# Kernel tuning notes

Hardware: AMD Instinct MI355X
Metric: run time of the kernel (lower is better)

The kernel has to match this reference:

```python
import jax, jax.numpy as jnp
import numpy as np

N = 131072
N_DIM = 128
NUM_LAYERS = 8
N_MID = NUM_LAYERS - 2  # middle (n_dim -> n_dim) layers


def _sigmoid_layer(h, u_un, w_un, log_a, b):
    # h: [N, in]; u_un: [out, in]; w_un: [out, out]; log_a, b: [out, 1]
    a = jnp.exp(log_a)                      # [out, 1]
    u = jax.nn.softmax(u_un, axis=1)        # row-softmax, matches Softmax(dim=1)
    w = jax.nn.softmax(w_un, axis=1)
    inner = h @ (a * u).T + b[:, 0]         # [N, out]
    return jax.nn.sigmoid(inner) @ w.T      # [N, out]


def setup_inputs() -> dict:
    key = jax.random.key(0)
    ks = jax.random.split(key, 24)
    d = N_DIM
    inp = {
        "x": jax.random.normal(ks[0], (N,), jnp.float32),
        "fy0": jax.random.normal(ks[1], (N,), jnp.float32),
        # first layer (in=2, out=d)
        "u0": jax.random.normal(ks[2], (d, 2), jnp.float32),
        "w0": jax.random.normal(ks[3], (d, d), jnp.float32),
        "la0": jax.random.normal(ks[4], (d, 1), jnp.float32),
        "b0": jax.random.normal(ks[5], (d, 1), jnp.float32),
        # middle layers stacked (in=d, out=d)
        "uM": jax.random.normal(ks[6], (N_MID, d, d), jnp.float32),
        "wM": jax.random.normal(ks[7], (N_MID, d, d), jnp.float32),
        "laM": jax.random.normal(ks[8], (N_MID, d, 1), jnp.float32),
        "bM": jax.random.normal(ks[9], (N_MID, d, 1), jnp.float32),
        # last layer (in=d, out=1)
        "uL": jax.random.normal(ks[10], (1, d), jnp.float32),
        "wL": jax.random.normal(ks[11], (1, 1), jnp.float32),
        "laL": jax.random.normal(ks[12], (1, 1), jnp.float32),
        "bL": jax.random.normal(ks[13], (1, 1), jnp.float32),
        # MLP 1 -> 50 -> 50 -> 1
        "W1": jax.random.normal(ks[14], (50, 1), jnp.float32) * 0.2,
        "b1": jax.random.normal(ks[15], (50,), jnp.float32) * 0.2,
        "W2": jax.random.normal(ks[16], (50, 50), jnp.float32) * 0.1,
        "b2": jax.random.normal(ks[17], (50,), jnp.float32) * 0.1,
        "W3": jax.random.normal(ks[18], (1, 50), jnp.float32) * 0.1,
        "b3": jax.random.normal(ks[19], (1,), jnp.float32) * 0.1,
    }
    return inp


def reference(x, fy0, u0, w0, la0, b0, uM, wM, laM, bM, uL, wL, laL, bL,
              W1, b1, W2, b2, W3, b3):
    # MLP feature net on fy0: [N,1] -> [N,1]
    h = jax.nn.relu(fy0[:, None] @ W1.T + b1)
    h = jax.nn.relu(h @ W2.T + b2)
    theta = h @ W3.T + b3                          # [N, 1]
    mono = jnp.concatenate([x[:, None], theta], 1)  # [N, 2]

    mono = _sigmoid_layer(mono, u0, w0, la0, b0)    # [N, d]

    def step(carry, p):
        u_un, w_un, log_a, b = p
        return _sigmoid_layer(carry, u_un, w_un, log_a, b), None

    mono, _ = jax.lax.scan(step, mono, (uM, wM, laM, bM))
    out = _sigmoid_layer(mono, uL, wL, laL, bL)     # [N, 1]
    return out[:, :, None]                          # [N, 1, 1] matches torch
```

## Files before the change

kernel.cpp:

```cpp
#include <hip/hip_runtime.h>
#include <cstdint>

typedef __attribute__((ext_vector_type(8))) _Float16 half8;
typedef __attribute__((ext_vector_type(16))) float f32x16;
typedef __attribute__((ext_vector_type(4))) float f4;

#define LOG2E 1.44269504088896340f
#define KNL  (-1.44269504088896340f)

__device__ __forceinline__ float fast_exp(float x) { return __builtin_amdgcn_exp2f(LOG2E * x); }
__device__ __forceinline__ float sigmoidf(float v) {
    return __builtin_amdgcn_rcpf(1.f + __builtin_amdgcn_exp2f(KNL * v));
}
__device__ __forceinline__ float sig2(float y) {
    return __builtin_amdgcn_rcpf(1.f + __builtin_amdgcn_exp2f(y));
}
__device__ __forceinline__ unsigned pkz(float a, float b) {
    return __builtin_bit_cast(unsigned, __builtin_amdgcn_cvt_pkrtz(a, b));
}
__device__ __forceinline__ void swapl(unsigned& a, unsigned& b) {
    asm volatile("v_permlane32_swap_b32 %0, %1" : "+v"(a), "+v"(b));
}
__device__ __forceinline__ void swaplf(float& a, float& b) {
    asm volatile("v_permlane32_swap_b32 %0, %1" : "+v"(a), "+v"(b));
}
union BU { unsigned u[4]; half8 h; };

constexpr int A0X = 0, A0T = 128, B0O = 256, BMO = 384, VLO = 1152,
              W1P = 1280, B1P = 1344, B2P = 1408, W3P = 1472, CN = 1536;

constexpr int LSTRIDE = 40960;
constexpr int GOFF  = 0;
constexpr int W2HIO = 6 * LSTRIDE;
constexpr int W2LOO = W2HIO + 8192;
constexpr int CGOFF = W2LOO + 8192;

__device__ __forceinline__ int rank_desc(const float* __restrict__ la, int i) {
    float mv = la[i];
    int r = 0;
    for (int j = 0; j < 128; ++j) {
        float v = la[j];
        r += (v > mv) || (v == mv && j < i);
    }
    return r;
}

__global__ __launch_bounds__(256)
void prep_kernel(const float* __restrict__ u0, const float* __restrict__ w0,
                 const float* __restrict__ la0, const float* __restrict__ b0,
                 const float* __restrict__ uM, const float* __restrict__ wM,
                 const float* __restrict__ laM, const float* __restrict__ bM,
                 const float* __restrict__ uL, const float* __restrict__ laL,
                 const float* __restrict__ W1, const float* __restrict__ b1,
                 const float* __restrict__ W2, const float* __restrict__ b2,
                 const float* __restrict__ W3,
                 char* __restrict__ G, _Float16* __restrict__ W2hi,
                 _Float16* __restrict__ W2lo, float* __restrict__ CgF)
{
    __shared__ float Wl[128 * 136];
    __shared__ float Al[8 * 132];
    __shared__ float uls[128];

    const int tid = threadIdx.x, b = blockIdx.x;
    const bool mblk = (b < 96);
    const int l = mblk ? (b >> 4) : 6;

    {
        const float* Wsrc = (l == 0) ? w0 : wM + (l - 1) * 16384;
        const int r = tid >> 1, h = tid & 1;
        const float* rp = Wsrc + r * 128 + h * 64;
        f4 buf[16];
#pragma unroll
        for (int v = 0; v < 16; ++v) buf[v] = *(const f4*)(rp + 4 * v);
        float mx = -1e30f;
#pragma unroll
        for (int v = 0; v < 16; ++v)
#pragma unroll
            for (int e = 0; e < 4; ++e) mx = fmaxf(mx, buf[v][e]);
        mx = fmaxf(mx, __shfl_xor(mx, 1));
        float s = 0.f;
#pragma unroll
        for (int v = 0; v < 16; ++v)
#pragma unroll
            for (int e = 0; e < 4; ++e) { buf[v][e] = fast_exp(buf[v][e] - mx); s += buf[v][e]; }
        s += __shfl_xor(s, 1);
        float inv = 1.f / s;
#pragma unroll
        for (int v = 0; v < 16; ++v)
            *(f4*)(&Wl[r * 136 + h * 64 + 4 * v]) = buf[v] * inv;
    }

    if (mblk) {
        const int q = b & 15;
        const int rl = tid >> 5, part = tid & 31;
        const int gi = q * 8 + rl;
        {
            f4 ub = *(const f4*)(uM + (l * 128 + gi) * 128 + part * 4);
            float mx = fmaxf(fmaxf(ub[0], ub[1]), fmaxf(ub[2], ub[3]));
#pragma unroll
            for (int o = 1; o < 32; o <<= 1) mx = fmaxf(mx, __shfl_xor(mx, o));
            float s = 0.f;
#pragma unroll
            for (int e = 0; e < 4; ++e) { ub[e] = fast_exp(ub[e] - mx); s += ub[e]; }
#pragma unroll
            for (int o = 1; o < 32; o <<= 1) s += __shfl_xor(s, o);
            float sc = fast_exp(laM[l * 128 + gi]) / s;
            *(f4*)(&Al[rl * 132 + part * 4]) = ub * sc;
        }
        __syncthreads();
        const int j0 = part * 4;
        f4 acc = {};
        for (int k = 0; k < 128; ++k) {
            float a = Al[rl * 132 + k];
            acc += a * *(const f4*)(&Wl[k * 136 + j0]);
        }
        const int rr = rank_desc(laM + l * 128, gi);
        int cs[4];
        if (l == 0) {
#pragma unroll
            for (int e = 0; e < 4; ++e) cs[e] = j0 + e;
        } else {
#pragma unroll
            for (int e = 0; e < 4; ++e) cs[e] = rank_desc(laM + (l - 1) * 128, j0 + e);
        }
        char* bh = G + l * LSTRIDE + rr * 256;
        char* bl = G + l * LSTRIDE + 32768 + rr * 256;
        const int sw = (rr & 7) << 4;
#pragma unroll
        for (int e = 0; e < 4; ++e) {
            float m = KNL * acc[e];
            _Float16 hh = (_Float16)m;
            *(_Float16*)(bh + ((2 * cs[e]) ^ sw)) = hh;
            if (rr < 32)
                *(_Float16*)(bl + ((2 * cs[e]) ^ sw)) = (_Float16)(m - (float)hh);
        }
        if (part == 0) CgF[BMO + l * 128 + rr] = KNL * bM[l * 128 + gi];
    } else {
        if (tid < 64) {
            float v0 = uL[tid], v1 = uL[tid + 64];
            float mx = fmaxf(v0, v1);
#pragma unroll
            for (int o = 32; o; o >>= 1) mx = fmaxf(mx, __shfl_xor(mx, o));
            float e0 = fast_exp(v0 - mx), e1 = fast_exp(v1 - mx);
            float ssum = e0 + e1;
#pragma unroll
            for (int o = 32; o; o >>= 1) ssum += __shfl_xor(ssum, o);
            float aL = fast_exp(laL[0]) / ssum;
            uls[tid]      = e0 * aL;
            uls[tid + 64] = e1 * aL;
        }
        __syncthreads();
        if (tid < 128) {
            float s = 0.f;
            for (int k = 0; k < 128; ++k) s += uls[k] * Wl[k * 136 + tid];
            CgF[VLO + rank_desc(laM + 5 * 128, tid)] = s;
        }
        if (tid < 128) {
            const int j = tid;
            float q0 = u0[2 * j], q1 = u0[2 * j + 1];
            float mx = fmaxf(q0, q1);
            float e0 = fast_exp(q0 - mx), e1 = fast_exp(q1 - mx);
            float a = fast_exp(la0[j]) / (e0 + e1);
            CgF[A0X + j] = KNL * a * e0;
            CgF[A0T + j] = KNL * a * e1;
            CgF[B0O + j] = KNL * b0[j];
        } else if (tid < 192) {
            const int t = tid - 128;
            CgF[W1P + t] = (t < 50) ? W1[t] : 0.f;
            CgF[B1P + t] = (t < 50) ? b1[t] : 0.f;
            CgF[B2P + t] = (t < 50) ? b2[t] : 0.f;
            CgF[W3P + t] = (t < 50) ? W3[t] : 0.f;
        }
        for (int i = tid; i < 4096; i += 256) {
            int r = i >> 6, c = i & 63;
            float v = (r < 50 && c < 50) ? W2[r * 50 + c] : 0.f;
            _Float16 h = (_Float16)v;
            W2hi[i] = h;
            W2lo[i] = (_Float16)(v - (float)h);
        }
    }
}


__device__ __forceinline__ void stage40(char* ls, const char* gs, int tid) {
#pragma unroll
    for (int i = 0; i < 10; ++i)
        __builtin_amdgcn_global_load_lds(
            (const __attribute__((address_space(1))) unsigned*)(uintptr_t)(gs + tid * 16 + i * 4096),
            (__attribute__((address_space(3))) unsigned*)(uintptr_t)(ls + tid * 16 + i * 4096),
            16, 0, 0);
}

__device__ __forceinline__ void epi_nt(const f32x16& a0, const f32x16& a1,
                                       half8& o00, half8& o01, half8& o10, half8& o11)
{
#pragma unroll
    for (int bt = 0; bt < 2; ++bt) {
        const f32x16& A = bt ? a1 : a0;
        unsigned p00 = pkz(sig2(A[0]),  sig2(A[1]));
        unsigned p01 = pkz(sig2(A[2]),  sig2(A[3]));
        unsigned p10 = pkz(sig2(A[4]),  sig2(A[5]));
        unsigned p11 = pkz(sig2(A[6]),  sig2(A[7]));
        unsigned p20 = pkz(sig2(A[8]),  sig2(A[9]));
        unsigned p21 = pkz(sig2(A[10]), sig2(A[11]));
        unsigned p30 = pkz(sig2(A[12]), sig2(A[13]));
        unsigned p31 = pkz(sig2(A[14]), sig2(A[15]));
        swapl(p00, p10); swapl(p01, p11);
        swapl(p20, p30); swapl(p21, p31);
        BU u0; u0.u[0] = p00; u0.u[1] = p01; u0.u[2] = p10; u0.u[3] = p11;
        BU u1; u1.u[0] = p20; u1.u[1] = p21; u1.u[2] = p30; u1.u[3] = p31;
        if (bt == 0) { o00 = u0.h; o01 = u1.h; }
        else         { o10 = u0.h; o11 = u1.h; }
    }
}

__device__ __forceinline__ void do_layer(const char* buf,
                                         const half8 (&Bin)[2][8], half8 (&Bout)[2][8],
                                         const float* __restrict__ biasK,
                                         int l31, int hi)
{
    const int sw = (l31 & 7) << 4;
#pragma unroll
    for (int nt = 0; nt < 4; ++nt) {
        f4 bv0 = *(const f4*)(biasK + 32 * nt + 4 * hi);
        f4 bv1 = *(const f4*)(biasK + 32 * nt + 8 + 4 * hi);
        f4 bv2 = *(const f4*)(biasK + 32 * nt + 16 + 4 * hi);
        f4 bv3 = *(const f4*)(biasK + 32 * nt + 24 + 4 * hi);
        f32x16 a0e = { bv0[0], bv0[1], bv0[2], bv0[3],
                       bv1[0], bv1[1], bv1[2], bv1[3],
                       bv2[0], bv2[1], bv2[2], bv2[3],
                       bv3[0], bv3[1], bv3[2], bv3[3] };
        f32x16 a1e = a0e;
        f32x16 a0o = {}, a1o = {};
        const char* rhi = buf + (nt * 32 + l31) * 256;
        __builtin_amdgcn_s_setprio(1);
#pragma unroll
        for (int ks = 0; ks < 8; ks += 2) {
            const int offE = (ks * 32 + hi * 16) ^ sw;
            const int offO = ((ks + 1) * 32 + hi * 16) ^ sw;
            half8 AhE = *(const half8*)(rhi + offE);
            half8 AhO = *(const half8*)(rhi + offO);
            a0e = __builtin_amdgcn_mfma_f32_32x32x16_f16(AhE, Bin[0][ks],     a0e, 0, 0, 0);
            a1e = __builtin_amdgcn_mfma_f32_32x32x16_f16(AhE, Bin[1][ks],     a1e, 0, 0, 0);
            a0o = __builtin_amdgcn_mfma_f32_32x32x16_f16(AhO, Bin[0][ks + 1], a0o, 0, 0, 0);
            a1o = __builtin_amdgcn_mfma_f32_32x32x16_f16(AhO, Bin[1][ks + 1], a1o, 0, 0, 0);
        }
        if (nt == 0) {
            const char* rlo = buf + 32768 + l31 * 256;
#pragma unroll
            for (int ks = 0; ks < 8; ks += 2) {
                const int offE = (ks * 32 + hi * 16) ^ sw;
                const int offO = ((ks + 1) * 32 + hi * 16) ^ sw;
                half8 AlE = *(const half8*)(rlo + offE);
                half8 AlO = *(const half8*)(rlo + offO);
                a0e = __builtin_amdgcn_mfma_f32_32x32x16_f16(AlE, Bin[0][ks],     a0e, 0, 0, 0);
                a1e = __builtin_amdgcn_mfma_f32_32x32x16_f16(AlE, Bin[1][ks],     a1e, 0, 0, 0);
                a0o = __builtin_amdgcn_mfma_f32_32x32x16_f16(AlO, Bin[0][ks + 1], a0o, 0, 0, 0);
                a1o = __builtin_amdgcn_mfma_f32_32x32x16_f16(AlO, Bin[1][ks + 1], a1o, 0, 0, 0);
            }
        }
        __builtin_amdgcn_s_setprio(0);
        f32x16 a0 = a0e + a0o, a1 = a1e + a1o;
        epi_nt(a0, a1, Bout[0][2 * nt], Bout[0][2 * nt + 1],
               Bout[1][2 * nt], Bout[1][2 * nt + 1]);
    }
}

__global__ __launch_bounds__(256, 2)
void mono_main(const float* __restrict__ x, const float* __restrict__ fy0,
               const char* __restrict__ G,
               const _Float16* __restrict__ W2hi, const _Float16* __restrict__ W2lo,
               const float* __restrict__ CgF, const float* __restrict__ b3g,
               const float* __restrict__ bLg, float* __restrict__ out)
{
    extern __shared__ __align__(16) char sm[];
    char* buf0 = sm;
    char* buf1 = sm + LSTRIDE;

    const int tid = threadIdx.x;
    const int lane = tid & 63, wave = tid >> 6;
    const int l31 = lane & 31, hi = lane >> 5;
    const int row0 = blockIdx.x * 256 + wave * 64;

    stage40(buf0, G, tid);
    const float b3s = b3g[0], bLs = bLg[0];

    float fy[2] = { fy0[row0 + l31], fy0[row0 + 32 + l31] };
    half8 Bm[2][4];
#pragma unroll
    for (int ks = 0; ks < 4; ++ks) {
        f4 w1a = *(const f4*)(CgF + W1P + 16 * ks + 8 * hi);
        f4 w1b = *(const f4*)(CgF + W1P + 16 * ks + 8 * hi + 4);
        f4 b1a = *(const f4*)(CgF + B1P + 16 * ks + 8 * hi);
        f4 b1b = *(const f4*)(CgF + B1P + 16 * ks + 8 * hi + 4);
#pragma unroll
        for (int bt = 0; bt < 2; ++bt) {
            BU u;
            u.u[0] = pkz(fmaxf(fy[bt] * w1a[0] + b1a[0], 0.f), fmaxf(fy[bt] * w1a[1] + b1a[1], 0.f));
            u.u[1] = pkz(fmaxf(fy[bt] * w1a[2] + b1a[2], 0.f), fmaxf(fy[bt] * w1a[3] + b1a[3], 0.f));
            u.u[2] = pkz(fmaxf(fy[bt] * w1b[0] + b1b[0], 0.f), fmaxf(fy[bt] * w1b[1] + b1b[1], 0.f));
            u.u[3] = pkz(fmaxf(fy[bt] * w1b[2] + b1b[2], 0.f), fmaxf(fy[bt] * w1b[3] + b1b[3], 0.f));
            Bm[bt][ks] = u.h;
        }
    }

    f32x16 a00 = {}, a01 = {}, a10 = {}, a11 = {};
#pragma unroll
    for (int nt = 0; nt < 2; ++nt)
#pragma unroll
        for (int ks = 0; ks < 4; ++ks) {
            half8 Ah = *(const half8*)(W2hi + (nt * 32 + l31) * 64 + ks * 16 + hi * 8);
            half8 Al = *(const half8*)(W2lo + (nt * 32 + l31) * 64 + ks * 16 + hi * 8);
            if (nt == 0) {
                a00 = __builtin_amdgcn_mfma_f32_32x32x16_f16(Ah, Bm[0][ks], a00, 0, 0, 0);
                a10 = __builtin_amdgcn_mfma_f32_32x32x16_f16(Ah, Bm[1][ks], a10, 0, 0, 0);
                a00 = __builtin_amdgcn_mfma_f32_32x32x16_f16(Al, Bm[0][ks], a00, 0, 0, 0);
                a10 = __builtin_amdgcn_mfma_f32_32x32x16_f16(Al, Bm[1][ks], a10, 0, 0, 0);
            } else {
                a01 = __builtin_amdgcn_mfma_f32_32x32x16_f16(Ah, Bm[0][ks], a01, 0, 0, 0);
                a11 = __builtin_amdgcn_mfma_f32_32x32x16_f16(Ah, Bm[1][ks], a11, 0, 0, 0);
                a01 = __builtin_amdgcn_mfma_f32_32x32x16_f16(Al, Bm[0][ks], a01, 0, 0, 0);
                a11 = __builtin_amdgcn_mfma_f32_32x32x16_f16(Al, Bm[1][ks], a11, 0, 0, 0);
            }
        }

    float tp0 = 0.f, tp1 = 0.f;
#pragma unroll
    for (int nt = 0; nt < 2; ++nt)
#pragma unroll
        for (int g = 0; g < 4; ++g) {
            f4 w3 = *(const f4*)(CgF + W3P + 32 * nt + 8 * g + 4 * hi);
            f4 b2v = *(const f4*)(CgF + B2P + 32 * nt + 8 * g + 4 * hi);
            const f32x16& A0 = nt ? a01 : a00;
            const f32x16& A1 = nt ? a11 : a10;
#pragma unroll
            for (int e = 0; e < 4; ++e) {
                tp0 += w3[e] * fmaxf(A0[4 * g + e] + b2v[e], 0.f);
                tp1 += w3[e] * fmaxf(A1[4 * g + e] + b2v[e], 0.f);
            }
        }
    swaplf(tp0, tp1);
    float th = tp0 + tp1 + b3s;
    float t0 = th, t1 = th;
    swaplf(t0, t1);

    float xr[2] = { x[row0 + l31], x[row0 + 32 + l31] };
    float thv[2] = { t0, t1 };
    half8 Bq[2][8], Bp[2][8];
#pragma unroll
    for (int ks = 0; ks < 8; ++ks) {
        f4 axa = *(const f4*)(CgF + A0X + 16 * ks + 8 * hi);
        f4 axb = *(const f4*)(CgF + A0X + 16 * ks + 8 * hi + 4);
        f4 ata = *(const f4*)(CgF + A0T + 16 * ks + 8 * hi);
        f4 atb = *(const f4*)(CgF + A0T + 16 * ks + 8 * hi + 4);
        f4 b0a = *(const f4*)(CgF + B0O + 16 * ks + 8 * hi);
        f4 b0b = *(const f4*)(CgF + B0O + 16 * ks + 8 * hi + 4);
#pragma unroll
        for (int bt = 0; bt < 2; ++bt) {
            BU u;
            u.u[0] = pkz(sig2(axa[0] * xr[bt] + ata[0] * thv[bt] + b0a[0]),
                         sig2(axa[1] * xr[bt] + ata[1] * thv[bt] + b0a[1]));
            u.u[1] = pkz(sig2(axa[2] * xr[bt] + ata[2] * thv[bt] + b0a[2]),
                         sig2(axa[3] * xr[bt] + ata[3] * thv[bt] + b0a[3]));
            u.u[2] = pkz(sig2(axb[0] * xr[bt] + atb[0] * thv[bt] + b0b[0]),
                         sig2(axb[1] * xr[bt] + atb[1] * thv[bt] + b0b[1]));
            u.u[3] = pkz(sig2(axb[2] * xr[bt] + atb[2] * thv[bt] + b0b[2]),
                         sig2(axb[3] * xr[bt] + atb[3] * thv[bt] + b0b[3]));
            Bq[bt][ks] = u.h;
        }
    }
    __syncthreads();

    stage40(buf1, G + 1 * LSTRIDE, tid);
    do_layer(buf0, Bq, Bp, CgF + BMO + 0 * 128, l31, hi);
    __syncthreads();
    stage40(buf0, G + 2 * LSTRIDE, tid);
    do_layer(buf1, Bp, Bq, CgF + BMO + 1 * 128, l31, hi);
    __syncthreads();
    stage40(buf1, G + 3 * LSTRIDE, tid);
    do_layer(buf0, Bq, Bp, CgF + BMO + 2 * 128, l31, hi);
    __syncthreads();
    stage40(buf0, G + 4 * LSTRIDE, tid);
    do_layer(buf1, Bp, Bq, CgF + BMO + 3 * 128, l31, hi);
    __syncthreads();
    stage40(buf1, G + 5 * LSTRIDE, tid);
    do_layer(buf0, Bq, Bp, CgF + BMO + 4 * 128, l31, hi);
    __syncthreads();
    do_layer(buf1, Bp, Bq, CgF + BMO + 5 * 128, l31, hi);

    float d0 = 0.f, d1 = 0.f;
#pragma unroll
    for (int ks = 0; ks < 8; ++ks) {
        f4 va = *(const f4*)(CgF + VLO + 16 * ks + 8 * hi);
        f4 vb = *(const f4*)(CgF + VLO + 16 * ks + 8 * hi + 4);
        half8 s0 = Bq[0][ks], s1 = Bq[1][ks];
#pragma unroll
        for (int e = 0; e < 4; ++e) {
            d0 += va[e] * (float)s0[e] + vb[e] * (float)s0[e + 4];
            d1 += va[e] * (float)s1[e] + vb[e] * (float)s1[e + 4];
        }
    }
    swaplf(d0, d1);
    out[row0 + lane] = sigmoidf(d0 + d1 + bLs);
}

extern "C" void kernel_launch(void* const* d_in, const int* in_sizes, int n_in,
                              void* d_out, int out_size, void* d_ws, size_t ws_size,
                              hipStream_t stream)
{
    const float* x   = (const float*)d_in[0];
    const float* fy0 = (const float*)d_in[1];
    const float* u0  = (const float*)d_in[2];
    const float* w0  = (const float*)d_in[3];
    const float* la0 = (const float*)d_in[4];
    const float* b0  = (const float*)d_in[5];
    const float* uM  = (const float*)d_in[6];
    const float* wM  = (const float*)d_in[7];
    const float* laM = (const float*)d_in[8];
    const float* bM  = (const float*)d_in[9];
    const float* uL  = (const float*)d_in[10];
    const float* laL = (const float*)d_in[12];
    const float* bL  = (const float*)d_in[13];
    const float* W1  = (const float*)d_in[14];
    const float* b1  = (const float*)d_in[15];
    const float* W2  = (const float*)d_in[16];
    const float* b2  = (const float*)d_in[17];
    const float* W3  = (const float*)d_in[18];
    const float* b3  = (const float*)d_in[19];
    float* out = (float*)d_out;

    char* ws = (char*)d_ws;
    char*     Gz   = ws + GOFF;
    _Float16* W2hi = (_Float16*)(ws + W2HIO);
    _Float16* W2lo = (_Float16*)(ws + W2LOO);
    float*    CgF  = (float*)(ws + CGOFF);

    prep_kernel<<<97, 256, 0, stream>>>(u0, w0, la0, b0, uM, wM, laM, bM,
                                        uL, laL, W1, b1, W2, b2, W3,
                                        Gz, W2hi, W2lo, CgF);

    static bool attr_set = false;
    if (!attr_set) {
        hipFuncSetAttribute((const void*)mono_main,
                            hipFuncAttributeMaxDynamicSharedMemorySize, 81920);
        attr_set = true;
    }
    mono_main<<<512, 256, 81920, stream>>>(x, fy0, Gz, W2hi, W2lo,
                                           CgF, b3, bL, out);
}
```

Measured before the change: 162.3 us.

## Use 512-thread blocks in main kernel and precompute rank slots in shared memory

The main kernel now launches 256 blocks of 512 threads (8 waves) instead of 512 blocks of 256, so each block's staged weights in LDS are shared by twice as many rows. The LDS staging loop is changed to match the larger block. In the prep kernel, the rank-sort slots for each block are computed once into shared memory rather than recomputed per thread. Risks: launch_bounds(512,4) is not achievable with 80KB LDS per block and may limit registers, and half as many blocks may leave CUs idle.

```diff
diff --git a/kernel.cpp b/kernel.cpp
--- a/kernel.cpp
+++ b/kernel.cpp
@@ -34,16 +34,6 @@
 constexpr int W2HIO = 6 * LSTRIDE;
 constexpr int W2LOO = W2HIO + 8192;
 constexpr int CGOFF = W2LOO + 8192;
-
-__device__ __forceinline__ int rank_desc(const float* __restrict__ la, int i) {
-    float mv = la[i];
-    int r = 0;
-    for (int j = 0; j < 128; ++j) {
-        float v = la[j];
-        r += (v > mv) || (v == mv && j < i);
-    }
-    return r;
-}
 
 __global__ __launch_bounds__(256)
 void prep_kernel(const float* __restrict__ u0, const float* __restrict__ w0,
@@ -60,10 +50,39 @@
     __shared__ float Wl[128 * 136];
     __shared__ float Al[8 * 132];
     __shared__ float uls[128];
+    __shared__ int rowSlot[128];
+    __shared__ int colSlot[128];
 
     const int tid = threadIdx.x, b = blockIdx.x;
     const bool mblk = (b < 96);
     const int l = mblk ? (b >> 4) : 6;
+
+    if (mblk) {
+        if (tid < 128) {
+            const float* laR = laM + l * 128;
+            float mv = laR[tid];
+            int r = 0;
+            for (int j = 0; j < 128; ++j) {
+                float v = laR[j];
+                r += (v > mv) || (v == mv && j < tid);
+            }
+            rowSlot[tid] = r;
+        } else {
+            const int t = tid - 128;
+            if (l > 0) {
+                const float* laC = laM + (l - 1) * 128;
+                float mv = laC[t];
+                int r = 0;
+                for (int j = 0; j < 128; ++j) {
+                    float v = laC[j];
+                    r += (v > mv) || (v == mv && j < t);
+                }
+                colSlot[t] = r;
+            } else {
+                colSlot[t] = t;
+            }
+        }
+    }
 
     {
         const float* Wsrc = (l == 0) ? w0 : wM + (l - 1) * 16384;
@@ -114,25 +133,18 @@
             float a = Al[rl * 132 + k];
             acc += a * *(const f4*)(&Wl[k * 136 + j0]);
         }
-        const int rr = rank_desc(laM + l * 128, gi);
-        int cs[4];
-        if (l == 0) {
-#pragma unroll
-            for (int e = 0; e < 4; ++e) cs[e] = j0 + e;
-        } else {
-#pragma unroll
-            for (int e = 0; e < 4; ++e) cs[e] = rank_desc(laM + (l - 1) * 128, j0 + e);
-        }
+        const int rr = rowSlot[gi];
         char* bh = G + l * LSTRIDE + rr * 256;
         char* bl = G + l * LSTRIDE + 32768 + rr * 256;
         const int sw = (rr & 7) << 4;
 #pragma unroll
         for (int e = 0; e < 4; ++e) {
+            const int cse = colSlot[j0 + e];
             float m = KNL * acc[e];
             _Float16 hh = (_Float16)m;
-            *(_Float16*)(bh + ((2 * cs[e]) ^ sw)) = hh;
+            *(_Float16*)(bh + ((2 * cse) ^ sw)) = hh;
             if (rr < 32)
-                *(_Float16*)(bl + ((2 * cs[e]) ^ sw)) = (_Float16)(m - (float)hh);
+                *(_Float16*)(bl + ((2 * cse) ^ sw)) = (_Float16)(m - (float)hh);
         }
         if (part == 0) CgF[BMO + l * 128 + rr] = KNL * bM[l * 128 + gi];
     } else {
@@ -153,7 +165,14 @@
         if (tid < 128) {
             float s = 0.f;
             for (int k = 0; k < 128; ++k) s += uls[k] * Wl[k * 136 + tid];
-            CgF[VLO + rank_desc(laM + 5 * 128, tid)] = s;
+            const float* la5 = laM + 5 * 128;
+            float mv = la5[tid];
+            int r = 0;
+            for (int j = 0; j < 128; ++j) {
+                float v = la5[j];
+                r += (v > mv) || (v == mv && j < tid);
+            }
+            CgF[VLO + r] = s;
         }
         if (tid < 128) {
             const int j = tid;
@@ -184,10 +203,10 @@
 
 __device__ __forceinline__ void stage40(char* ls, const char* gs, int tid) {
 #pragma unroll
-    for (int i = 0; i < 10; ++i)
+    for (int i = 0; i < 5; ++i)
         __builtin_amdgcn_global_load_lds(
-            (const __attribute__((address_space(1))) unsigned*)(uintptr_t)(gs + tid * 16 + i * 4096),
-            (__attribute__((address_space(3))) unsigned*)(uintptr_t)(ls + tid * 16 + i * 4096),
+            (const __attribute__((address_space(1))) unsigned*)(uintptr_t)(gs + tid * 16 + i * 8192),
+            (__attribute__((address_space(3))) unsigned*)(uintptr_t)(ls + tid * 16 + i * 8192),
             16, 0, 0);
 }
 
@@ -266,7 +285,7 @@
     }
 }
 
-__global__ __launch_bounds__(256, 2)
+__global__ __launch_bounds__(512, 4)
 void mono_main(const float* __restrict__ x, const float* __restrict__ fy0,
                const char* __restrict__ G,
                const _Float16* __restrict__ W2hi, const _Float16* __restrict__ W2lo,
@@ -280,7 +299,7 @@
     const int tid = threadIdx.x;
     const int lane = tid & 63, wave = tid >> 6;
     const int l31 = lane & 31, hi = lane >> 5;
-    const int row0 = blockIdx.x * 256 + wave * 64;
+    const int row0 = blockIdx.x * 512 + wave * 64;
 
     stage40(buf0, G, tid);
     const float b3s = b3g[0], bLs = bLg[0];
@@ -445,6 +464,6 @@
                             hipFuncAttributeMaxDynamicSharedMemorySize, 81920);
         attr_set = true;
     }
-    mono_main<<<512, 256, 81920, stream>>>(x, fy0, Gz, W2hi, W2lo,
+    mono_main<<<256, 512, 81920, stream>>>(x, fy0, Gz, W2hi, W2lo,
                                            CgF, b3, bL, out);
 }
```

After: 233.7 us. +44.0%, slower.
